# Kernel optimization log

Hardware: AMD Instinct MI355X
Metric: run time of the kernel (lower is better)

Reference implementation:

```python
import jax, jax.numpy as jnp
import numpy as np

DEST = 64          # args['output_size']
NET = 256          # network_size = input_size - 3*dest_size
INPUT = NET + 3 * DEST  # 448
B, N = 4, 2048


def setup_inputs() -> dict:
    key = jax.random.key(0)
    ks = jax.random.split(key, 9)
    node_feature = jax.random.normal(ks[0], (B, N, INPUT), jnp.float32)
    adj_forward = jax.random.uniform(ks[1], (B, N, N), jnp.float32)
    adj_backward = jax.random.uniform(ks[2], (B, N, N), jnp.float32)
    s = 1.0 / np.sqrt(2 * DEST)
    Wf = jax.random.normal(ks[3], (2 * DEST, DEST), jnp.float32) * s
    bf = jnp.zeros((DEST,), jnp.float32)
    Wb = jax.random.normal(ks[4], (2 * DEST, DEST), jnp.float32) * s
    bb = jnp.zeros((DEST,), jnp.float32)
    W_emb = jax.random.normal(ks[5], (NET, 2 * DEST), jnp.float32) / np.sqrt(NET)
    b_emb = jnp.zeros((2 * DEST,), jnp.float32)
    return {"node_feature": node_feature, "adj_forward": adj_forward,
            "adj_backward": adj_backward, "Wf": Wf, "bf": bf,
            "Wb": Wb, "bb": bb, "W_emb": W_emb, "b_emb": b_emb}


def _gcn(x, adj, W, b):
    # GCN layer: aggregate neighbors then project. x: [B,N,2d], adj: [B,N,N]
    h = jnp.einsum('bmn,bnf->bmf', adj, x)  # message passing
    return h @ W + b                         # [B,N,d]


def reference(node_feature, adj_forward, adj_backward, Wf, bf, Wb, bb, W_emb, b_emb):
    dyn = node_feature[:, :, :DEST]                 # [B,N,d]
    struct = node_feature[:, :, DEST:3 * DEST]      # [B,N,2d]
    stat = node_feature[:, :, 3 * DEST:]            # [B,N,NET]
    fwd_code = dyn * _gcn(struct, adj_forward, Wf, bf)
    bwd_code = dyn * _gcn(struct, adj_backward, Wb, bb)
    emb = jnp.concatenate((fwd_code, bwd_code), axis=2)  # [B,N,2d]
    gate = jax.nn.sigmoid(stat @ W_emb + b_emb)           # [B,N,2d]
    return emb * gate
```

## Files before the change

kernel.cpp:

```cpp
#include <hip/hip_runtime.h>
#include <hip/hip_bf16.h>
#include <math.h>

#define BB   4
#define NN   2048
#define INPT 448

typedef float f32x4 __attribute__((ext_vector_type(4)));
typedef short s16x8 __attribute__((ext_vector_type(8)));
typedef unsigned int u32;

#define MFMA(a,b,c) __builtin_amdgcn_mfma_f32_16x16x32_bf16((a),(b),(c),0,0,0)

__device__ __align__(16) unsigned short g_WcatF[4*8*64*8];
__device__ __align__(16) unsigned short g_WembF[8*8*64*8];
__device__ __align__(16) unsigned short g_UtF[BB*2*64*4*64*8];
__device__ __align__(16) float          g_G2[BB*NN*128];

__device__ __forceinline__ u32 bf16pk(float a, float b) {
    u32 ua = __builtin_bit_cast(u32, a);
    u32 ub = __builtin_bit_cast(u32, b);
    ua += 0x7fffu + ((ua >> 16) & 1u);
    ub += 0x7fffu + ((ub >> 16) & 1u);
    return (ua >> 16) | (ub & 0xffff0000u);
}
__device__ __forceinline__ unsigned short bf16b(float a) {
    u32 ua = __builtin_bit_cast(u32, a);
    ua += 0x7fffu + ((ua >> 16) & 1u);
    return (unsigned short)(ua >> 16);
}

__global__ void k_weights(const float* __restrict__ Wf, const float* __restrict__ Wb,
                          const float* __restrict__ We) {
    int t = blockIdx.x * 256 + threadIdx.x;
    if (t < 2048) {
        int l = t & 63, jf = (t >> 6) & 7, kg = t >> 9;
        int j  = jf * 16 + (l & 15);
        int f0 = kg * 32 + (l >> 4) * 8;
        union { u32 u[4]; s16x8 s; } r;
        #pragma unroll
        for (int e = 0; e < 8; e += 2) {
            float v0 = (j < 64) ? Wf[(f0 + e    ) * 64 + j] : Wb[(f0 + e    ) * 64 + (j - 64)];
            float v1 = (j < 64) ? Wf[(f0 + e + 1) * 64 + j] : Wb[(f0 + e + 1) * 64 + (j - 64)];
            r.u[e >> 1] = bf16pk(v0, v1);
        }
        *(s16x8*)&g_WcatF[t * 8] = r.s;
    } else if (t < 2048 + 4096) {
        int idx = t - 2048;
        int l = idx & 63, cf = (idx >> 6) & 7, kg = idx >> 9;
        int c  = cf * 16 + (l & 15);
        int k0 = kg * 32 + (l >> 4) * 8;
        union { u32 u[4]; s16x8 s; } r;
        #pragma unroll
        for (int e = 0; e < 8; e += 2)
            r.u[e >> 1] = bf16pk(We[(k0 + e) * 128 + c], We[(k0 + e + 1) * 128 + c]);
        *(s16x8*)&g_WembF[idx * 8] = r.s;
    }
}

__global__ __launch_bounds__(256) void k_prep(const float* __restrict__ nfeat,
                                              const float* __restrict__ bemb) {
    __shared__ __align__(16) char sm[24576];
    int tid = threadIdx.x;
    int w = tid >> 6, l = tid & 63, lr = l & 15, lc = l >> 4;
    int bid = blockIdx.x;

    if (bid < 256) {
        int b = bid >> 6, nb = bid & 63;
        unsigned short* ss = (unsigned short*)sm;
        unsigned short* ob = (unsigned short*)(sm + 8192);
        const float* base = nfeat + (size_t)(b * NN + nb * 32) * INPT;
        #pragma unroll
        for (int i = 0; i < 4; ++i) {
            int node = w * 8 + i * 2 + (l >> 5);
            int c4 = (l & 31) * 4;
            float4 v = *(const float4*)(base + (size_t)node * INPT + 64 + c4);
            int off = node * 256 + c4 * 2; off ^= (node & 7) << 4;
            uint2 pk; pk.x = bf16pk(v.x, v.y); pk.y = bf16pk(v.z, v.w);
            *(uint2*)((char*)ss + off) = pk;
        }
        __syncthreads();
        f32x4 acc[2][2] = {};
        #pragma unroll
        for (int kg = 0; kg < 4; ++kg) {
            s16x8 a0 = *(const s16x8*)&g_WcatF[((kg * 8 + w * 2 + 0) * 64 + l) * 8];
            s16x8 a1 = *(const s16x8*)&g_WcatF[((kg * 8 + w * 2 + 1) * 64 + l) * 8];
            #pragma unroll
            for (int na = 0; na < 2; ++na) {
                int off = (na * 16 + lr) * 256 + kg * 64 + lc * 16; off ^= (lr & 7) << 4;
                s16x8 bf = *(const s16x8*)((char*)ss + off);
                acc[0][na] = MFMA(a0, bf, acc[0][na]);
                acc[1][na] = MFMA(a1, bf, acc[1][na]);
            }
        }
        #pragma unroll
        for (int ja = 0; ja < 2; ++ja)
            #pragma unroll
            for (int na = 0; na < 2; ++na)
                #pragma unroll
                for (int r = 0; r < 4; ++r) {
                    int j = w * 32 + ja * 16 + lc * 4 + r;
                    int n = na * 16 + lr;
                    ob[j * 32 + n] = bf16b(acc[ja][na][r]);
                }
        __syncthreads();
        #pragma unroll
        for (int q = 0; q < 2; ++q) {
            int idx = q * 256 + tid;
            int dirx = idx >> 8, nf = (idx >> 6) & 3, ll = idx & 63;
            int j = dirx * 64 + nf * 16 + (ll & 15);
            int n0 = (ll >> 4) * 8;
            s16x8 v = *(const s16x8*)&ob[j * 32 + n0];
            *(s16x8*)&g_UtF[((((size_t)(b * 2 + dirx) * 64 + nb) * 4 + nf) * 64 + ll) * 8] = v;
        }
    } else {
        int bid2 = bid - 256;
        int b = bid2 >> 6, mb = bid2 & 63;
        unsigned short* ss = (unsigned short*)sm;
        float* dyls = (float*)(sm + 16384);
        const float* base = nfeat + (size_t)(b * NN + mb * 32) * INPT;
        #pragma unroll
        for (int i = 0; i < 8; ++i) {
            int row = w * 8 + i;
            float4 v = *(const float4*)(base + (size_t)row * INPT + 192 + l * 4);
            int off = row * 512 + l * 8; off ^= (row & 7) << 4;
            uint2 pk; pk.x = bf16pk(v.x, v.y); pk.y = bf16pk(v.z, v.w);
            *(uint2*)((char*)ss + off) = pk;
        }
        #pragma unroll
        for (int i = 0; i < 2; ++i) {
            int row = w * 8 + i * 4 + lc;
            float4 v = *(const float4*)(base + (size_t)row * INPT + lr * 4);
            *(float4*)&dyls[row * 64 + lr * 4] = v;
        }
        __syncthreads();
        f32x4 acc[2][2] = {};
        #pragma unroll
        for (int kg = 0; kg < 8; ++kg) {
            s16x8 a0, a1;
            {
                int off = lr * 512 + kg * 64 + lc * 16; off ^= (lr & 7) << 4;
                a0 = *(const s16x8*)((char*)ss + off);
                a1 = *(const s16x8*)((char*)ss + off + 8192);
            }
            #pragma unroll
            for (int cfi = 0; cfi < 2; ++cfi) {
                s16x8 bf = *(const s16x8*)&g_WembF[((kg * 8 + w * 2 + cfi) * 64 + l) * 8];
                acc[cfi][0] = MFMA(a0, bf, acc[cfi][0]);
                acc[cfi][1] = MFMA(a1, bf, acc[cfi][1]);
            }
        }
        #pragma unroll
        for (int cfi = 0; cfi < 2; ++cfi) {
            int c = (w * 2 + cfi) * 16 + lr;
            float be = bemb[c];
            #pragma unroll
            for (int mf = 0; mf < 2; ++mf)
                #pragma unroll
                for (int r = 0; r < 4; ++r) {
                    int m = mf * 16 + lc * 4 + r;
                    float v = acc[cfi][mf][r] + be;
                    float g = 1.0f / (1.0f + expf(-v));
                    g_G2[(size_t)(b * NN + mb * 32 + m) * 128 + c] = g * dyls[m * 64 + (c & 63)];
                }
        }
    }
}

__global__ __launch_bounds__(512, 8) void k_main(const float* __restrict__ adjf,
                                                 const float* __restrict__ adjb,
                                                 const float* __restrict__ biasf,
                                                 const float* __restrict__ biasb,
                                                 float* __restrict__ out) {
    __shared__ __align__(16) char sm[32768];
    int tid = threadIdx.x;
    int w = tid >> 6, l = tid & 63, lr = l & 15, lc = l >> 4;
    int bid = blockIdx.x;
    int tile = bid & 127, dir = (bid >> 7) & 1, b = bid >> 8;
    const float* adj  = dir ? adjb : adjf;
    const float* bias = dir ? biasb : biasf;
    int m0 = tile * 16;
    const unsigned short* utF = g_UtF + (size_t)(b * 2 + dir) * 131072;
    const float* ag = adj + (size_t)(b * NN + m0) * NN + w * 256;
    char* abase = sm + w * 4096;

    float4 av[16];
    #pragma unroll
    for (int c = 0; c < 4; ++c)
        #pragma unroll
        for (int i = 0; i < 4; ++i)
            av[c * 4 + i] = *(const float4*)(ag + (size_t)(4 * i + lc) * NN + c * 64 + (l & 15) * 4);

    f32x4 acc[4] = {};
    #pragma unroll
    for (int c = 0; c < 4; ++c) {
        char* abuf = abase + (c & 1) * 2048;
        #pragma unroll
        for (int i = 0; i < 4; ++i) {
            int row = 4 * i + lc;
            int off = row * 128 + (l & 15) * 8; off ^= (row & 7) << 4;
            uint2 pk;
            pk.x = bf16pk(av[c * 4 + i].x, av[c * 4 + i].y);
            pk.y = bf16pk(av[c * 4 + i].z, av[c * 4 + i].w);
            *(uint2*)(abuf + off) = pk;
        }
        #pragma unroll
        for (int ii = 0; ii < 2; ++ii) {
            int off = lr * 128 + ii * 64 + lc * 16; off ^= (lr & 7) << 4;
            s16x8 af = *(const s16x8*)(abuf + off);
            int kk = w * 8 + c * 2 + ii;
            #pragma unroll
            for (int nf = 0; nf < 4; ++nf) {
                s16x8 bf = *(const s16x8*)&utF[((kk * 4 + nf) * 64 + l) * 8];
                acc[nf] = MFMA(af, bf, acc[nf]);
            }
        }
    }

    float* red = (float*)sm;
    __syncthreads();
    #pragma unroll
    for (int nf = 0; nf < 4; ++nf)
        #pragma unroll
        for (int r = 0; r < 4; ++r)
            red[(w * 16 + nf * 4 + r) * 64 + l] = acc[nf][r];
    __syncthreads();
    if (w < 4) {
        #pragma unroll
        for (int r = 0; r < 4; ++r) {
            float s = 0.f;
            #pragma unroll
            for (int wp = 0; wp < 8; ++wp)
                s += red[(wp * 16 + w * 4 + r) * 64 + l];
            int col = w * 16 + lr;
            int m = m0 + lc * 4 + r;
            size_t o = (size_t)(b * NN + m) * 128 + dir * 64 + col;
            out[o] = (s + bias[col]) * g_G2[o];
        }
    }
}

extern "C" void kernel_launch(void* const* d_in, const int* in_sizes, int n_in,
                              void* d_out, int out_size, void* d_ws, size_t ws_size,
                              hipStream_t stream) {
    (void)in_sizes; (void)n_in; (void)d_ws; (void)ws_size; (void)out_size;
    const float* nfeat = (const float*)d_in[0];
    const float* adjf  = (const float*)d_in[1];
    const float* adjb  = (const float*)d_in[2];
    const float* Wf    = (const float*)d_in[3];
    const float* bf    = (const float*)d_in[4];
    const float* Wb    = (const float*)d_in[5];
    const float* bb    = (const float*)d_in[6];
    const float* We    = (const float*)d_in[7];
    const float* bemb  = (const float*)d_in[8];
    float* out = (float*)d_out;

    hipLaunchKernelGGL(k_weights, dim3(24),   dim3(256), 0, stream, Wf, Wb, We);
    hipLaunchKernelGGL(k_prep,    dim3(512),  dim3(256), 0, stream, nfeat, bemb);
    hipLaunchKernelGGL(k_main,    dim3(1024), dim3(512), 0, stream, adjf, adjb, bf, bb, out);
}
```

Before: 190.6 us.

## Restructure GCN main kernel into double-buffered K loop with LDS-staged weights

The main kernel changes from 512 threads, each wave owning a K slice and finishing with a cross-wave LDS reduction, to 256 threads that walk the full K range in 32 steps. Each step prefetches the next adjacency and weight tile with inline-asm global loads into double-buffered LDS, so loads overlap the MFMAs and the reduction disappears. It also remaps the block index so consecutive hardware blocks are spread across batch and direction. The costs are a barrier on every step and fewer waves per block, since each wave now handles only one 16-column output slice.

```diff
diff --git a/kernel.cpp b/kernel.cpp
--- a/kernel.cpp
+++ b/kernel.cpp
@@ -167,76 +167,86 @@
     }
 }
 
-__global__ __launch_bounds__(512, 8) void k_main(const float* __restrict__ adjf,
-                                                 const float* __restrict__ adjb,
-                                                 const float* __restrict__ biasf,
-                                                 const float* __restrict__ biasb,
-                                                 float* __restrict__ out) {
-    __shared__ __align__(16) char sm[32768];
+#define GLOAD(dst, p) \
+    asm volatile("global_load_dwordx4 %0, %1, off" : "=v"(dst) : "v"(p) : "memory")
+
+__global__ __launch_bounds__(256) void k_main(const float* __restrict__ adjf,
+                                              const float* __restrict__ adjb,
+                                              const float* __restrict__ biasf,
+                                              const float* __restrict__ biasb,
+                                              float* __restrict__ out) {
+    __shared__ __align__(16) char sm[20480];
     int tid = threadIdx.x;
     int w = tid >> 6, l = tid & 63, lr = l & 15, lc = l >> 4;
-    int bid = blockIdx.x;
+
+    int hw  = blockIdx.x;
+    int bid = (hw & 7) * 128 + (hw >> 3);
     int tile = bid & 127, dir = (bid >> 7) & 1, b = bid >> 8;
+
     const float* adj  = dir ? adjb : adjf;
     const float* bias = dir ? biasb : biasf;
     int m0 = tile * 16;
     const unsigned short* utF = g_UtF + (size_t)(b * 2 + dir) * 131072;
-    const float* ag = adj + (size_t)(b * NN + m0) * NN + w * 256;
-    char* abase = sm + w * 4096;
-
-    float4 av[16];
+
+    int arow = tid >> 4;
+    int u8   = tid & 15;
+    const float* asrc = adj + (size_t)(b * NN + m0 + arow) * NN + u8 * 4;
+    int awoff = arow * 128 + ((((u8 >> 1) ^ (arow & 7)) << 4)) + (u8 & 1) * 8;
+    const unsigned short* bs0 = utF + (size_t)w * 512 + l * 8;
+    const unsigned short* bs1 = bs0 + 2048;
+    int boff0 = (w * 64 + l) * 16;
+    int boff1 = ((4 + w) * 64 + l) * 16;
+
+    f32x4 acc = {};
+
+    {
+        f32x4 a0, bv0, bv1;
+        GLOAD(a0, asrc);
+        GLOAD(bv0, bs0);
+        GLOAD(bv1, bs1);
+        asm volatile("s_waitcnt vmcnt(0)" : "+v"(a0), "+v"(bv0), "+v"(bv1) : : "memory");
+        uint2 pk; pk.x = bf16pk(a0[0], a0[1]); pk.y = bf16pk(a0[2], a0[3]);
+        *(uint2*)(sm + awoff) = pk;
+        *(f32x4*)(sm + 4096 + boff0) = bv0;
+        *(f32x4*)(sm + 4096 + boff1) = bv1;
+    }
+    __syncthreads();
+
+    for (int t = 0; t < 32; ++t) {
+        f32x4 an, bn0, bn1;
+        bool pre = (t < 31);
+        if (pre) {
+            GLOAD(an,  asrc + (t + 1) * 64);
+            GLOAD(bn0, bs0 + (t + 1) * 4096);
+            GLOAD(bn1, bs1 + (t + 1) * 4096);
+        }
+        char* Ab = sm + (t & 1) * 2048;
+        char* Bb = sm + 4096 + (t & 1) * 8192;
+        #pragma unroll
+        for (int kk = 0; kk < 2; ++kk) {
+            s16x8 af = *(const s16x8*)(Ab + lr * 128 + (((kk * 4 + lc) ^ (lr & 7)) << 4));
+            s16x8 bf = *(const s16x8*)(Bb + ((kk * 4 + w) * 64 + l) * 16);
+            acc = MFMA(af, bf, acc);
+        }
+        if (pre) {
+            asm volatile("s_waitcnt vmcnt(0)" : "+v"(an), "+v"(bn0), "+v"(bn1) : : "memory");
+            char* Ab2 = sm + ((t + 1) & 1) * 2048;
+            char* Bb2 = sm + 4096 + ((t + 1) & 1) * 8192;
+            uint2 pk; pk.x = bf16pk(an[0], an[1]); pk.y = bf16pk(an[2], an[3]);
+            *(uint2*)(Ab2 + awoff) = pk;
+            *(f32x4*)(Bb2 + boff0) = bn0;
+            *(f32x4*)(Bb2 + boff1) = bn1;
+        }
+        __syncthreads();
+    }
+
+    int col = w * 16 + lr;
+    float bv = bias[col];
     #pragma unroll
-    for (int c = 0; c < 4; ++c)
-        #pragma unroll
-        for (int i = 0; i < 4; ++i)
-            av[c * 4 + i] = *(const float4*)(ag + (size_t)(4 * i + lc) * NN + c * 64 + (l & 15) * 4);
-
-    f32x4 acc[4] = {};
-    #pragma unroll
-    for (int c = 0; c < 4; ++c) {
-        char* abuf = abase + (c & 1) * 2048;
-        #pragma unroll
-        for (int i = 0; i < 4; ++i) {
-            int row = 4 * i + lc;
-            int off = row * 128 + (l & 15) * 8; off ^= (row & 7) << 4;
-            uint2 pk;
-            pk.x = bf16pk(av[c * 4 + i].x, av[c * 4 + i].y);
-            pk.y = bf16pk(av[c * 4 + i].z, av[c * 4 + i].w);
-            *(uint2*)(abuf + off) = pk;
-        }
-        #pragma unroll
-        for (int ii = 0; ii < 2; ++ii) {
-            int off = lr * 128 + ii * 64 + lc * 16; off ^= (lr & 7) << 4;
-            s16x8 af = *(const s16x8*)(abuf + off);
-            int kk = w * 8 + c * 2 + ii;
-            #pragma unroll
-            for (int nf = 0; nf < 4; ++nf) {
-                s16x8 bf = *(const s16x8*)&utF[((kk * 4 + nf) * 64 + l) * 8];
-                acc[nf] = MFMA(af, bf, acc[nf]);
-            }
-        }
-    }
-
-    float* red = (float*)sm;
-    __syncthreads();
-    #pragma unroll
-    for (int nf = 0; nf < 4; ++nf)
-        #pragma unroll
-        for (int r = 0; r < 4; ++r)
-            red[(w * 16 + nf * 4 + r) * 64 + l] = acc[nf][r];
-    __syncthreads();
-    if (w < 4) {
-        #pragma unroll
-        for (int r = 0; r < 4; ++r) {
-            float s = 0.f;
-            #pragma unroll
-            for (int wp = 0; wp < 8; ++wp)
-                s += red[(wp * 16 + w * 4 + r) * 64 + l];
-            int col = w * 16 + lr;
-            int m = m0 + lc * 4 + r;
-            size_t o = (size_t)(b * NN + m) * 128 + dir * 64 + col;
-            out[o] = (s + bias[col]) * g_G2[o];
-        }
+    for (int r = 0; r < 4; ++r) {
+        int mrow = m0 + lc * 4 + r;
+        size_t o = (size_t)(b * NN + mrow) * 128 + dir * 64 + col;
+        out[o] = (acc[r] + bv) * g_G2[o];
     }
 }
 
@@ -257,5 +267,5 @@
 
     hipLaunchKernelGGL(k_weights, dim3(24),   dim3(256), 0, stream, Wf, Wb, We);
     hipLaunchKernelGGL(k_prep,    dim3(512),  dim3(256), 0, stream, nfeat, bemb);
-    hipLaunchKernelGGL(k_main,    dim3(1024), dim3(512), 0, stream, adjf, adjb, bf, bb, out);
-}
+    hipLaunchKernelGGL(k_main,    dim3(1024), dim3(256), 0, stream, adjf, adjb, bf, bb, out);
+}
```

Measured after the change: 183.7 us. 3.6% less time.
